# Performance work log

Hardware: AMD Instinct MI355X
Metric: run time of the kernel (lower is better)

Reference implementation:

```python
import jax, jax.numpy as jnp
import numpy as np

N = 50000   # nodes
E = 800000  # edges
H = 4       # heads
FH = 32     # hidden per head
C = 40      # classes
IN = 128    # input feats
EPS = 1e-5
NEG_SLOPE = 0.2


def setup_inputs() -> dict:
    key = jax.random.key(0)
    ks = jax.random.split(key, 32)
    rn = lambda k, s, sc=0.1: jax.random.normal(k, s, jnp.float32) * sc
    return {
        "feat": rn(ks[0], (N, IN), 1.0),
        "src": jax.random.randint(ks[1], (E,), 0, N, jnp.int32),
        "dst": jax.random.randint(ks[2], (E,), 0, N, jnp.int32),
        "w_fc0": rn(ks[3], (IN, H * FH)), "al0": rn(ks[4], (H, FH)), "ar0": rn(ks[5], (H, FH)),
        "b0": jnp.zeros((H * FH,), jnp.float32), "w_lin0": rn(ks[6], (IN, H * FH)),
        "g0": jnp.ones((H * FH,), jnp.float32), "be0": jnp.zeros((H * FH,), jnp.float32),
        "w_fc1": rn(ks[7], (H * FH, H * FH)), "al1": rn(ks[8], (H, FH)), "ar1": rn(ks[9], (H, FH)),
        "b1": jnp.zeros((H * FH,), jnp.float32), "w_lin1": rn(ks[10], (H * FH, H * FH)),
        "g1": jnp.ones((H * FH,), jnp.float32), "be1": jnp.zeros((H * FH,), jnp.float32),
        "w_fc2": rn(ks[11], (H * FH, H * C)), "al2": rn(ks[12], (H, C)), "ar2": rn(ks[13], (H, C)),
        "b2": jnp.zeros((H * C,), jnp.float32), "w_lin2": rn(ks[14], (H * FH, H * C)),
        "bias_last": jnp.zeros((C,), jnp.float32),
    }


def gat_layer(h, src, dst, w_fc, al, ar, b, w_lin, out_f):
    # h: [N, in]; ft: [N, H, out_f]
    ft = (h @ w_fc).reshape(N, H, out_f)
    el = jnp.einsum("nhf,hf->nh", ft, al)   # [N, H]
    er = jnp.einsum("nhf,hf->nh", ft, ar)   # [N, H]
    e = jax.nn.leaky_relu(el[src] + er[dst], NEG_SLOPE)  # [E, H]
    # segment softmax over destination neighborhoods
    m = jax.ops.segment_max(e, dst, num_segments=N)       # [N, H]
    ex = jnp.exp(e - m[dst])
    s = jax.ops.segment_sum(ex, dst, num_segments=N)      # [N, H]
    a = ex / s[dst]                                       # [E, H]
    msg = ft[src] * a[:, :, None]                         # [E, H, out_f]
    rst = jax.ops.segment_sum(msg, dst, num_segments=N)   # [N, H, out_f]
    rst = rst + b.reshape(1, H, out_f)
    skip = (h @ w_lin).reshape(N, H, out_f)
    return rst + skip


def batchnorm(x, g, be):
    mu = jnp.mean(x, axis=0)
    var = jnp.mean(jnp.square(x - mu), axis=0)
    return (x - mu) * jax.lax.rsqrt(var + EPS) * g + be


def reference(feat, src, dst,
              w_fc0, al0, ar0, b0, w_lin0, g0, be0,
              w_fc1, al1, ar1, b1, w_lin1, g1, be1,
              w_fc2, al2, ar2, b2, w_lin2, bias_last):
    h = feat
    h = gat_layer(h, src, dst, w_fc0, al0, ar0, b0, w_lin0, FH).reshape(N, H * FH)
    h = jax.nn.relu(batchnorm(h, g0, be0))
    h = gat_layer(h, src, dst, w_fc1, al1, ar1, b1, w_lin1, FH).reshape(N, H * FH)
    h = jax.nn.relu(batchnorm(h, g1, be1))
    h = gat_layer(h, src, dst, w_fc2, al2, ar2, b2, w_lin2, C)  # [N, H, C]
    h = h.mean(axis=1) + bias_last
    return jax.nn.log_softmax(h, axis=-1)
```

## Files before the change

kernel.cpp:

```cpp
#include <hip/hip_runtime.h>
#include <hip/hip_bf16.h>

#define GN 50000
#define GE 800000
#define GH 4
#define GFH 32
#define GC 40
#define GIN 128

typedef __hip_bfloat16 bf16;
typedef __attribute__((ext_vector_type(8))) short bf16x8;
typedef __attribute__((ext_vector_type(4))) float f32x4;

static __device__ __forceinline__ float ldx(const void* p, size_t i, int m) {
    if (m) return ((const float*)p)[i];
    return __bfloat162float(((const bf16*)p)[i]);
}
static __device__ __forceinline__ void stx(void* p, size_t i, int m, float v) {
    if (m) ((float*)p)[i] = v;
    else ((bf16*)p)[i] = __float2bfloat16(v);
}
static __device__ __forceinline__ unsigned short f2bfu(float v) {
    union { bf16 b; unsigned short u; } cv;
    cv.b = __float2bfloat16(v);
    return cv.u;
}
static __device__ __forceinline__ float lo16(unsigned u) { return __uint_as_float(u << 16); }
static __device__ __forceinline__ float hi16(unsigned u) { return __uint_as_float(u & 0xFFFF0000u); }
static __device__ __forceinline__ float guard_finite(float v) {
    if (!(v == v) || fabsf(v) > 1e30f) return 0.f;
    return v;
}

__global__ void detect_kernel(const unsigned short* __restrict__ f, int* __restrict__ flag) {
    int t = threadIdx.x;
    unsigned short u = f[t];
    int e = (u >> 7) & 0xFF;
    if (e >= 0x8E) atomicAdd(flag, 1);
}

__global__ void sentinel_kernel(unsigned short* __restrict__ o, int n) {
    int i = blockIdx.x * blockDim.x + threadIdx.x;
    if (i < n) o[i] = 0x3F80;
}

__global__ void count_kernel(const int* __restrict__ dst, int* __restrict__ deg, int n) {
    int e = blockIdx.x * blockDim.x + threadIdx.x;
    if (e < n) {
        int d = dst[e];
        if (d >= 0 && d < GN) atomicAdd(&deg[d], 1);
    }
}

__global__ void scan1_kernel(const int* __restrict__ deg, int* __restrict__ tmp,
                             int* __restrict__ bsum, int n) {
    int tid = threadIdx.x;
    int i = blockIdx.x * 256 + tid;
    int v = (i < n) ? deg[i] : 0;
    int lane = tid & 63, wid = tid >> 6;
    int s = v;
#pragma unroll
    for (int off = 1; off < 64; off <<= 1) {
        int u = __shfl_up(s, off);
        if (lane >= off) s += u;
    }
    __shared__ int wsum[4];
    if (lane == 63) wsum[wid] = s;
    __syncthreads();
    int woff = 0;
#pragma unroll
    for (int w = 0; w < 4; w++) woff += (w < wid) ? wsum[w] : 0;
    int incl = s + woff;
    if (i < n) tmp[i] = incl;
    if (tid == 255) bsum[blockIdx.x] = incl;
}

__global__ void scan2_kernel(int* __restrict__ bsum, int nb) {
    int tid = threadIdx.x;
    int v = (tid < nb) ? bsum[tid] : 0;
    int lane = tid & 63, wid = tid >> 6;
    int s = v;
#pragma unroll
    for (int off = 1; off < 64; off <<= 1) {
        int u = __shfl_up(s, off);
        if (lane >= off) s += u;
    }
    __shared__ int wsum[4];
    if (lane == 63) wsum[wid] = s;
    __syncthreads();
    int woff = 0;
#pragma unroll
    for (int w = 0; w < 4; w++) woff += (w < wid) ? wsum[w] : 0;
    if (tid < nb) bsum[tid] = s + woff - v;
}

__global__ void scan3_kernel(const int* __restrict__ deg, const int* __restrict__ tmp,
                             const int* __restrict__ bsum, int* __restrict__ indptr,
                             int* __restrict__ cursor, int n) {
    int i = blockIdx.x * 256 + threadIdx.x;
    if (i < n) {
        int incl = tmp[i] + bsum[blockIdx.x];
        indptr[i + 1] = incl;
        cursor[i] = incl - deg[i];
        if (i == 0) indptr[0] = 0;
    }
}

__global__ void scatter_kernel(const int* __restrict__ src, const int* __restrict__ dst,
                               int* __restrict__ cursor, int* __restrict__ csr_src, int n) {
    int e = blockIdx.x * blockDim.x + threadIdx.x;
    if (e < n) {
        int d = dst[e];
        if (d < 0 || d >= GN) return;
        int p = atomicAdd(&cursor[d], 1);
        if (p >= 0 && p < GE) csr_src[p] = src[e];
    }
}

__global__ void wmean_kernel(const void* __restrict__ w, unsigned short* __restrict__ wmt,
                             const int* __restrict__ flag) {
    int m = (*flag != 0) ? 1 : 0;
    int idx = blockIdx.x * blockDim.x + threadIdx.x;
    if (idx < 48 * 128) {
        int c = idx >> 7, k = idx & 127;
        float s = 0.f;
        if (c < 40) {
            s = 0.25f * (ldx(w, (size_t)k * 160 + c, m) + ldx(w, (size_t)k * 160 + 40 + c, m) +
                         ldx(w, (size_t)k * 160 + 80 + c, m) + ldx(w, (size_t)k * 160 + 120 + c, m));
        }
        wmt[c * 128 + k] = f2bfu(s);
    }
}

__global__ void wtrans_all(const void* __restrict__ wf0, const void* __restrict__ wl0,
                           const void* __restrict__ wf1, const void* __restrict__ wl1,
                           const void* __restrict__ wf2, unsigned short* __restrict__ tf0,
                           unsigned short* __restrict__ tl0, unsigned short* __restrict__ tf1,
                           unsigned short* __restrict__ tl1, unsigned short* __restrict__ tf2,
                           const int* __restrict__ flag) {
    int m = (*flag != 0) ? 1 : 0;
    int idx = blockIdx.x * blockDim.x + threadIdx.x;
    if (idx < 4 * 16384) {
        int which = idx >> 14, local = idx & 16383;
        const void* w = (which == 0) ? wf0 : (which == 1) ? wl0 : (which == 2) ? wf1 : wl1;
        unsigned short* t = (which == 0) ? tf0 : (which == 1) ? tl0 : (which == 2) ? tf1 : tl1;
        int c = local & 127, k = local >> 7;
        t[(size_t)c * 128 + k] = f2bfu(ldx(w, (size_t)k * 128 + c, m));
    } else if (idx < 4 * 16384 + 160 * 128) {
        int local = idx - 4 * 16384;
        int c = local % 160, k = local / 160;
        tf2[(size_t)c * 128 + k] = f2bfu(ldx(wf2, (size_t)k * 160 + c, m));
    }
}

__global__ void bn_coef(const float* __restrict__ gsum, const float* __restrict__ gsq,
                        const void* __restrict__ g, const void* __restrict__ be,
                        float* __restrict__ ka, float* __restrict__ kb, int n,
                        const int* __restrict__ flag) {
    int c = threadIdx.x;
    int m = (*flag != 0) ? 1 : 0;
    float inv_n = 1.f / (float)n;
    float mu = gsum[c] * inv_n;
    float var = gsq[c] * inv_n - mu * mu;
    float k = rsqrtf(fmaxf(var, 0.f) + 1e-5f) * ldx(g, c, m);
    ka[c] = k;
    kb[c] = ldx(be, c, m) - mu * k;
}

static __device__ __forceinline__ uint4 bnx8(uint4 v, int k0, const float* __restrict__ ka,
                                             const float* __restrict__ kb) {
    unsigned* pw = (unsigned*)&v;
#pragma unroll
    for (int j = 0; j < 4; j++) {
        int c = k0 + 2 * j;
        float y0 = fmaf(lo16(pw[j]), ka[c], kb[c]);
        float y1 = fmaf(hi16(pw[j]), ka[c + 1], kb[c + 1]);
        y0 = y0 > 0.f ? y0 : 0.f;
        y1 = y1 > 0.f ? y1 : 0.f;
        pw[j] = (unsigned)f2bfu(y0) | ((unsigned)f2bfu(y1) << 16);
    }
    return v;
}

__global__ __launch_bounds__(256) void gemm_dual(const void* __restrict__ X, int xext,
                                                 const unsigned short* __restrict__ WT1,
                                                 const unsigned short* __restrict__ WT2,
                                                 bf16* __restrict__ Y1, bf16* __restrict__ Y2,
                                                 int nrows, const float* __restrict__ ka,
                                                 const float* __restrict__ kb,
                                                 const void* __restrict__ al,
                                                 const void* __restrict__ ar,
                                                 float* __restrict__ elo,
                                                 float* __restrict__ ero,
                                                 const int* __restrict__ flag) {
    constexpr int LDX = 136;
    __shared__ unsigned short Xs[64 * LDX];
    __shared__ unsigned short Wt[128 * LDX];
    int m = (*flag != 0) ? 1 : 0;
    int xfp32 = xext && m;
    int tid = threadIdx.x;
    int rb = blockIdx.x * 64;

    if (xfp32) {
#pragma unroll
        for (int it = 0; it < 8; it++) {
            int e = (tid + it * 256) * 4;
            int r = e >> 7, k0 = e & 127;
            int row = rb + r;
            float4 v = {0.f, 0.f, 0.f, 0.f};
            if (row < nrows) v = *(const float4*)((const float*)X + (size_t)row * 128 + k0);
            unsigned lo = (unsigned)f2bfu(v.x) | ((unsigned)f2bfu(v.y) << 16);
            unsigned hi = (unsigned)f2bfu(v.z) | ((unsigned)f2bfu(v.w) << 16);
            uint2 o = {lo, hi};
            *(uint2*)&Xs[r * LDX + k0] = o;
        }
    } else {
#pragma unroll
        for (int it = 0; it < 4; it++) {
            int e = (tid + it * 256) * 8;
            int r = e >> 7, k0 = e & 127;
            int row = rb + r;
            uint4 v = {0u, 0u, 0u, 0u};
            if (row < nrows) v = *(const uint4*)((const unsigned short*)X + (size_t)row * 128 + k0);
            if (ka) v = bnx8(v, k0, ka, kb);
            *(uint4*)&Xs[r * LDX + k0] = v;
        }
    }
#pragma unroll
    for (int it = 0; it < 8; it++) {
        int e = (tid + it * 256) * 8;
        int c = e >> 7, k0 = e & 127;
        *(uint4*)&Wt[c * LDX + k0] = *(const uint4*)(WT1 + (size_t)c * 128 + k0);
    }
    __syncthreads();

    int wave = tid >> 6, lane = tid & 63;
    int lr = lane & 15, quad = lane >> 4;
    int mrow = wave * 16 + lr;
    int drow = rb + wave * 16 + quad * 4;

    {
        f32x4 acc[8] = {};
        for (int kk = 0; kk < 128; kk += 32) {
            bf16x8 a = *(const bf16x8*)&Xs[mrow * LDX + kk + quad * 8];
#pragma unroll
            for (int nt = 0; nt < 8; nt++) {
                bf16x8 b = *(const bf16x8*)&Wt[(nt * 16 + lr) * LDX + kk + quad * 8];
                acc[nt] = __builtin_amdgcn_mfma_f32_16x16x32_bf16(a, b, acc[nt], 0, 0, 0);
            }
        }
#pragma unroll
        for (int nt = 0; nt < 8; nt++) {
            int col = nt * 16 + lr;
#pragma unroll
            for (int i = 0; i < 4; i++) {
                int row = drow + i;
                if (row < nrows) Y1[(size_t)row * 128 + col] = __float2bfloat16(acc[nt][i]);
            }
        }
        float alv[8], arv[8];
#pragma unroll
        for (int nt = 0; nt < 8; nt++) {
            int c = nt * 16 + lr;
            alv[nt] = ldx(al, c, m);
            arv[nt] = ldx(ar, c, m);
        }
        float eo = 0.f, ro = 0.f;
#pragma unroll
        for (int i = 0; i < 4; i++) {
#pragma unroll
            for (int h = 0; h < 4; h++) {
                float es = acc[2 * h][i] * alv[2 * h] + acc[2 * h + 1][i] * alv[2 * h + 1];
                float rs = acc[2 * h][i] * arv[2 * h] + acc[2 * h + 1][i] * arv[2 * h + 1];
#pragma unroll
                for (int off = 1; off < 16; off <<= 1) {
                    es += __shfl_xor(es, off);
                    rs += __shfl_xor(rs, off);
                }
                bool mine = (lr == i * 4 + h);
                eo = mine ? es : eo;
                ro = mine ? rs : ro;
            }
        }
        int erow = drow + (lr >> 2);
        if (erow < nrows) {
            elo[(size_t)drow * 4 + lr] = eo;
            ero[(size_t)drow * 4 + lr] = ro;
        }
    }
    __syncthreads();
#pragma unroll
    for (int it = 0; it < 8; it++) {
        int e = (tid + it * 256) * 8;
        int c = e >> 7, k0 = e & 127;
        *(uint4*)&Wt[c * LDX + k0] = *(const uint4*)(WT2 + (size_t)c * 128 + k0);
    }
    __syncthreads();
    {
        f32x4 acc[8] = {};
        for (int kk = 0; kk < 128; kk += 32) {
            bf16x8 a = *(const bf16x8*)&Xs[mrow * LDX + kk + quad * 8];
#pragma unroll
            for (int nt = 0; nt < 8; nt++) {
                bf16x8 b = *(const bf16x8*)&Wt[(nt * 16 + lr) * LDX + kk + quad * 8];
                acc[nt] = __builtin_amdgcn_mfma_f32_16x16x32_bf16(a, b, acc[nt], 0, 0, 0);
            }
        }
#pragma unroll
        for (int nt = 0; nt < 8; nt++) {
            int col = nt * 16 + lr;
#pragma unroll
            for (int i = 0; i < 4; i++) {
                int row = drow + i;
                if (row < nrows) Y2[(size_t)row * 128 + col] = __float2bfloat16(acc[nt][i]);
            }
        }
    }
}

__global__ __launch_bounds__(256) void gemm_final(bf16* __restrict__ X,
                                                  const unsigned short* __restrict__ WT,
                                                  bf16* __restrict__ Y, int nrows,
                                                  const float* __restrict__ ka,
                                                  const float* __restrict__ kb) {
    constexpr int LDX = 136;
    __shared__ unsigned short Xs[64 * LDX];
    __shared__ unsigned short Wt[128 * LDX];
    int tid = threadIdx.x;
    int rb = blockIdx.x * 64;

#pragma unroll
    for (int it = 0; it < 4; it++) {
        int e = (tid + it * 256) * 8;
        int r = e >> 7, k0 = e & 127;
        int row = rb + r;
        uint4 v = {0u, 0u, 0u, 0u};
        if (row < nrows) v = *(const uint4*)((const unsigned short*)X + (size_t)row * 128 + k0);
        v = bnx8(v, k0, ka, kb);
        *(uint4*)&Xs[r * LDX + k0] = v;
    }
#pragma unroll
    for (int it = 0; it < 8; it++) {
        int e = (tid + it * 256) * 8;
        int c = e >> 7, k0 = e & 127;
        *(uint4*)&Wt[c * LDX + k0] = *(const uint4*)(WT + (size_t)c * 128 + k0);
    }
    __syncthreads();

    int wave = tid >> 6, lane = tid & 63;
    int lr = lane & 15, quad = lane >> 4;
    int mrow = wave * 16 + lr;
    int drow = rb + wave * 16 + quad * 4;

    {
        f32x4 acc[8] = {};
        for (int kk = 0; kk < 128; kk += 32) {
            bf16x8 a = *(const bf16x8*)&Xs[mrow * LDX + kk + quad * 8];
#pragma unroll
            for (int nt = 0; nt < 8; nt++) {
                bf16x8 b = *(const bf16x8*)&Wt[(nt * 16 + lr) * LDX + kk + quad * 8];
                acc[nt] = __builtin_amdgcn_mfma_f32_16x16x32_bf16(a, b, acc[nt], 0, 0, 0);
            }
        }
#pragma unroll
        for (int nt = 0; nt < 8; nt++) {
            int col = nt * 16 + lr;
#pragma unroll
            for (int i = 0; i < 4; i++) {
                int row = drow + i;
                if (row < nrows) Y[(size_t)row * 160 + col] = __float2bfloat16(acc[nt][i]);
            }
        }
    }
    __syncthreads();
#pragma unroll
    for (int it = 0; it < 5; it++) {
        int e = (tid + it * 256) * 8;
        int c = e >> 7, k0 = e & 127;
        *(uint4*)&Wt[c * LDX + k0] = *(const uint4*)(WT + (size_t)(128 + c) * 128 + k0);
    }
    __syncthreads();
    {
        f32x4 acc[5] = {};
        for (int kk = 0; kk < 128; kk += 32) {
            bf16x8 a = *(const bf16x8*)&Xs[mrow * LDX + kk + quad * 8];
#pragma unroll
            for (int nt = 0; nt < 5; nt++) {
                bf16x8 b = *(const bf16x8*)&Wt[(nt * 16 + lr) * LDX + kk + quad * 8];
                acc[nt] = __builtin_amdgcn_mfma_f32_16x16x32_bf16(a, b, acc[nt], 0, 0, 0);
            }
        }
#pragma unroll
        for (int nt = 0; nt < 5; nt++) {
            int colg = 128 + nt * 16 + lr;
#pragma unroll
            for (int i = 0; i < 4; i++) {
                int row = drow + i;
                if (row >= nrows) continue;
                if (colg < 160) {
                    Y[(size_t)row * 160 + colg] = __float2bfloat16(acc[nt][i]);
                } else {
                    int sc = colg - 160;
                    if (sc < 40) X[(size_t)row * 128 + sc] = __float2bfloat16(acc[nt][i]);
                }
            }
        }
    }
}

__global__ void elr_kernel(const bf16* __restrict__ ft, const void* __restrict__ al,
                           const void* __restrict__ ar, float* __restrict__ el,
                           float* __restrict__ er, int n, int F, const int* __restrict__ flag) {
    int m = (*flag != 0) ? 1 : 0;
    int gid = blockIdx.x * blockDim.x + threadIdx.x;
    if (gid >= n * 4) return;
    int nid = gid >> 2, h = gid & 3;
    const bf16* f = ft + (size_t)nid * (4 * F) + h * F;
    float sl = 0.f, sr = 0.f;
    for (int i0 = 0; i0 < F; i0 += 8) {
        bf16x8 v8 = *(const bf16x8*)(f + i0);
#pragma unroll
        for (int i = 0; i < 8; i++) {
            float v = __uint_as_float(((unsigned)(unsigned short)v8[i]) << 16);
            sl += v * ldx(al, h * F + i0 + i, m);
            sr += v * ldx(ar, h * F + i0 + i, m);
        }
    }
    el[gid] = sl;
    er[gid] = sr;
}

template <int FTOT, bool FINAL>
__global__ __launch_bounds__(256) void agg_wave(
    const bf16* __restrict__ ft, const float* __restrict__ el, const float* __restrict__ er,
    const int* __restrict__ indptr, const int* __restrict__ csr_src,
    const void* __restrict__ bias, const void* __restrict__ h_in,
    const bf16* __restrict__ skip_pre, bf16* __restrict__ out,
    const void* __restrict__ bias_last, void* __restrict__ fout,
    const int* __restrict__ flag) {
    constexpr int HF = FTOT / 4;
    int m = (*flag != 0) ? 1 : 0;
    int lane = threadIdx.x & 63;
    int v = blockIdx.x * 4 + (threadIdx.x >> 6);
    if (v >= GN) return;
    int beg = indptr[v], end = indptr[v + 1];
    beg = max(0, min(beg, GE));
    end = max(beg, min(end, GE));

    int h = lane & 3, jl = lane >> 2;
    int c0 = 2 * lane;
    int h0 = c0 / HF;
    float erv = er[v * 4 + h];

    float a0 = 0.f, a1 = 0.f, a2 = 0.f, a3 = 0.f;
    float s_part = 0.f;

    for (int cb = beg; cb < end; cb += 16) {
        int chn = end - cb;
        chn = chn < 16 ? chn : 16;
        int u = csr_src[cb + (jl < chn ? jl : chn - 1)];
        u = min(max(u, 0), GN - 1);
        float e = el[u * 4 + h] + erv;
        e = e > 0.f ? e : 0.2f * e;
        float w = (jl < chn) ? __expf(fminf(e, 60.f)) : 0.f;
        s_part += w;
#pragma unroll
        for (int jb = 0; jb < 16; jb += 8) {
            if (jb >= chn) break;
            unsigned pq[8];
            float wqv[8];
            unsigned pbq[8];
#pragma unroll
            for (int q = 0; q < 8; q++) {
                int j4 = (jb + q) * 4;
                int us = __builtin_amdgcn_readlane(u, j4);
                pq[q] = *(const unsigned*)(ft + (size_t)us * FTOT + c0);
                wqv[q] = __shfl(w, j4 + h0);
                if constexpr (FINAL) {
                    if (lane < 16) {
                        pbq[q] = *(const unsigned*)(ft + (size_t)us * FTOT + 128 + c0);
                    }
                }
            }
#pragma unroll
            for (int q = 0; q < 8; q++) {
                a0 += wqv[q] * lo16(pq[q]);
                a1 += wqv[q] * hi16(pq[q]);
                if constexpr (FINAL) {
                    float wb = __uint_as_float(
                        __builtin_amdgcn_readlane(__float_as_uint(w), (jb + q) * 4 + 3));
                    if (lane < 16) {
                        a2 += wb * lo16(pbq[q]);
                        a3 += wb * hi16(pbq[q]);
                    }
                }
            }
        }
    }

#pragma unroll
    for (int off = 4; off < 64; off <<= 1) s_part += __shfl_xor(s_part, off);
    float s0 = __shfl(s_part, h0);

    float r0 = (s0 > 0.f) ? a0 / s0 : 0.f;
    float r1 = (s0 > 0.f) ? a1 / s0 : 0.f;

    if constexpr (!FINAL) {
        unsigned pk = *(const unsigned*)(skip_pre + (size_t)v * FTOT + c0);
        float o0 = r0 + ldx(bias, c0, m) + lo16(pk);
        float o1 = r1 + ldx(bias, c0 + 1, m) + hi16(pk);
        unsigned po = ((unsigned)f2bfu(guard_finite(o1)) << 16) |
                      (unsigned)f2bfu(guard_finite(o0));
        *(unsigned*)(out + (size_t)v * FTOT + c0) = po;
    } else {
        float s3 = __shfl(s_part, 3);
        float o0 = r0 + ldx(bias, c0, m);
        float o1 = r1 + ldx(bias, c0 + 1, m);
        float r2 = (s3 > 0.f) ? a2 / s3 : 0.f;
        float r3 = (s3 > 0.f) ? a3 / s3 : 0.f;
        int cb0 = 128 + c0;
        float o2 = r2 + ldx(bias, (cb0 < FTOT) ? cb0 : 0, m);
        float o3 = r3 + ldx(bias, (cb0 + 1 < FTOT) ? cb0 + 1 : 1, m);

        int t = lane;
        bool od = (t & 1);
        int sA = (t >> 1) & 63;
        int sB = ((t + 40) >> 1) & 63;
        int sC = ((t + 80) >> 1) & 63;
        int sD1 = ((t + 120) >> 1) & 63;
        int sD2 = ((t >= 8 ? t - 8 : 0) >> 1);
        float vA0 = __shfl(o0, sA), vA1 = __shfl(o1, sA);
        float vB0 = __shfl(o0, sB), vB1 = __shfl(o1, sB);
        float vC0 = __shfl(o0, sC), vC1 = __shfl(o1, sC);
        float vD10 = __shfl(o0, sD1), vD11 = __shfl(o1, sD1);
        float vD20 = __shfl(o2, sD2), vD21 = __shfl(o3, sD2);
        float vA = od ? vA1 : vA0;
        float vB = od ? vB1 : vB0;
        float vC = od ? vC1 : vC0;
        float vD = (t < 8) ? (od ? vD11 : vD10) : (od ? vD21 : vD20);

        float x = -3.0e38f;
        if (t < 40) {
            float sm = __bfloat162float(((const bf16*)h_in)[(size_t)v * 128 + t]);
            x = 0.25f * (vA + vB + vC + vD) + sm + ldx(bias_last, t, m);
        }
        float mx = x;
#pragma unroll
        for (int off = 1; off < 64; off <<= 1) mx = fmaxf(mx, __shfl_xor(mx, off));
        float ex = (t < 40) ? __expf(x - mx) : 0.f;
        float sum = ex;
#pragma unroll
        for (int off = 1; off < 64; off <<= 1) sum += __shfl_xor(sum, off);
        if (t < 40) stx(fout, (size_t)v * 40 + t, m, guard_finite(x - mx - __logf(sum)));
    }
}

__global__ void bn_stats(const bf16* __restrict__ x, float* __restrict__ gsum,
                         float* __restrict__ gsq, int n) {
    __shared__ float ls[128], lq[128];
    int tid = threadIdx.x;
    if (tid < 128) {
        ls[tid] = 0.f;
        lq[tid] = 0.f;
    }
    __syncthreads();
    int rg = tid >> 4;
    int c8 = (tid & 15) * 8;
    int rows_per_block = (n + gridDim.x - 1) / gridDim.x;
    int r0 = blockIdx.x * rows_per_block;
    int r1 = min(n, r0 + rows_per_block);
    float s[8] = {}, q[8] = {};
    for (int r = r0 + rg; r < r1; r += 16) {
        uint4 v = *(const uint4*)((const unsigned short*)x + (size_t)r * 128 + c8);
        unsigned* pw = (unsigned*)&v;
#pragma unroll
        for (int i = 0; i < 4; i++) {
            float v0 = lo16(pw[i]), v1 = hi16(pw[i]);
            s[2 * i] += v0;
            q[2 * i] += v0 * v0;
            s[2 * i + 1] += v1;
            q[2 * i + 1] += v1 * v1;
        }
    }
#pragma unroll
    for (int i = 0; i < 8; i++) {
        atomicAdd(&ls[c8 + i], s[i]);
        atomicAdd(&lq[c8 + i], q[i]);
    }
    __syncthreads();
    if (tid < 128) {
        atomicAdd(&gsum[tid], ls[tid]);
        atomicAdd(&gsq[tid], lq[tid]);
    }
}

extern "C" void kernel_launch(void* const* d_in, const int* in_sizes, int n_in,
                              void* d_out, int out_size, void* d_ws, size_t ws_size,
                              hipStream_t stream) {
    const void* feat = d_in[0];
    const int* src = (const int*)d_in[1];
    const int* dst = (const int*)d_in[2];
    const void* w_fc0 = d_in[3];
    const void* al0 = d_in[4];
    const void* ar0 = d_in[5];
    const void* b0 = d_in[6];
    const void* w_lin0 = d_in[7];
    const void* g0 = d_in[8];
    const void* be0 = d_in[9];
    const void* w_fc1 = d_in[10];
    const void* al1 = d_in[11];
    const void* ar1 = d_in[12];
    const void* b1 = d_in[13];
    const void* w_lin1 = d_in[14];
    const void* g1 = d_in[15];
    const void* be1 = d_in[16];
    const void* w_fc2 = d_in[17];
    const void* al2 = d_in[18];
    const void* ar2 = d_in[19];
    const void* b2 = d_in[20];
    const void* w_lin2 = d_in[21];
    const void* bias_last = d_in[22];

    if (ws_size < 35000000) {
        sentinel_kernel<<<(out_size + 255) / 256, 256, 0, stream>>>((unsigned short*)d_out,
                                                                    out_size);
        return;
    }

    char* p = (char*)d_ws;
    auto alloc = [&](size_t bytes) {
        char* r = p;
        p += (bytes + 255) & ~(size_t)255;
        return r;
    };
    bf16* ftb = (bf16*)alloc((size_t)GN * 160 * 2);
    bf16* hbuf = (bf16*)alloc((size_t)GN * 128 * 2);
    float* elb = (float*)alloc((size_t)GN * 4 * 4);
    float* erb = (float*)alloc((size_t)GN * 4 * 4);
    int* indptr = (int*)alloc((size_t)(GN + 1) * 4);
    int* cursor = (int*)alloc((size_t)GN * 4);
    int* bsum = (int*)alloc(256 * 4);
    unsigned short* wtf0 = (unsigned short*)alloc(128 * 128 * 2);
    unsigned short* wtl0 = (unsigned short*)alloc(128 * 128 * 2);
    unsigned short* wtf1 = (unsigned short*)alloc(128 * 128 * 2);
    unsigned short* wtl1 = (unsigned short*)alloc(128 * 128 * 2);
    unsigned short* wtf2 = (unsigned short*)alloc(208 * 128 * 2);
    float* ka0 = (float*)alloc(128 * 4);
    float* kb0 = (float*)alloc(128 * 4);
    float* ka1 = (float*)alloc(128 * 4);
    float* kb1 = (float*)alloc(128 * 4);
    char* zbase = p;
    int* deg = (int*)alloc((size_t)GN * 4);
    int* csr = (int*)alloc((size_t)GE * 4);
    float* gs0 = (float*)alloc(128 * 4);
    float* gq0 = (float*)alloc(128 * 4);
    float* gs1 = (float*)alloc(128 * 4);
    float* gq1 = (float*)alloc(128 * 4);
    int* flag = (int*)alloc(4);
    hipMemsetAsync(zbase, 0, (size_t)(p - zbase), stream);

    unsigned short* wmt = wtf2 + 160 * 128;

    detect_kernel<<<1, 256, 0, stream>>>((const unsigned short*)feat, flag);

    const int NB = (GN + 255) / 256;
    count_kernel<<<(GE + 255) / 256, 256, 0, stream>>>(dst, deg, GE);
    scan1_kernel<<<NB, 256, 0, stream>>>(deg, cursor, bsum, GN);
    scan2_kernel<<<1, 256, 0, stream>>>(bsum, NB);
    scan3_kernel<<<NB, 256, 0, stream>>>(deg, cursor, bsum, indptr, cursor, GN);
    scatter_kernel<<<(GE + 255) / 256, 256, 0, stream>>>(src, dst, cursor, csr, GE);
    wmean_kernel<<<24, 256, 0, stream>>>(w_lin2, wmt, flag);
    wtrans_all<<<(4 * 16384 + 160 * 128 + 255) / 256, 256, 0, stream>>>(
        w_fc0, w_lin0, w_fc1, w_lin1, w_fc2, wtf0, wtl0, wtf1, wtl1, wtf2, flag);

    const int AGGB = (GN + 3) / 4;

    gemm_dual<<<782, 256, 0, stream>>>(feat, 1, wtf0, wtl0, ftb, hbuf, GN, nullptr, nullptr,
                                       al0, ar0, elb, erb, flag);
    agg_wave<128, false><<<AGGB, 256, 0, stream>>>(ftb, elb, erb, indptr, csr, b0, nullptr,
                                                   hbuf, hbuf, nullptr, nullptr, flag);
    bn_stats<<<256, 256, 0, stream>>>(hbuf, gs0, gq0, GN);
    bn_coef<<<1, 128, 0, stream>>>(gs0, gq0, g0, be0, ka0, kb0, GN, flag);

    gemm_dual<<<782, 256, 0, stream>>>(hbuf, 0, wtf1, wtl1, ftb, hbuf, GN, ka0, kb0,
                                       al1, ar1, elb, erb, flag);
    agg_wave<128, false><<<AGGB, 256, 0, stream>>>(ftb, elb, erb, indptr, csr, b1, nullptr,
                                                   hbuf, hbuf, nullptr, nullptr, flag);
    bn_stats<<<256, 256, 0, stream>>>(hbuf, gs1, gq1, GN);
    bn_coef<<<1, 128, 0, stream>>>(gs1, gq1, g1, be1, ka1, kb1, GN, flag);

    gemm_final<<<782, 256, 0, stream>>>(hbuf, wtf2, ftb, GN, ka1, kb1);
    elr_kernel<<<(GN * 4 + 255) / 256, 256, 0, stream>>>(ftb, al2, ar2, elb, erb, GN, 40, flag);
    agg_wave<160, true><<<AGGB, 256, 0, stream>>>(ftb, elb, erb, indptr, csr, b2, hbuf,
                                                  nullptr, nullptr, bias_last, d_out, flag);
}
```

Baseline: 440.6 us.

## Fold small kernels together, preconvert features, and prefetch GEMM weights into registers

Merges the w_lin2 mean computation into the weight transpose kernel. Folds the BatchNorm coefficient computation into bn_stats with a last-block-done counter, removing separate tiny launches. Adds a standalone feature-to-bf16 conversion kernel written into ftb, so gemm_dual always reads bf16 input. Both GEMMs now issue all X and weight global loads into registers up front before the LDS stores, which overlaps load latency at the cost of higher register pressure and an extra pass over the features.

```diff
diff --git a/kernel.cpp b/kernel.cpp
--- a/kernel.cpp
+++ b/kernel.cpp
@@ -42,6 +42,26 @@
 __global__ void sentinel_kernel(unsigned short* __restrict__ o, int n) {
     int i = blockIdx.x * blockDim.x + threadIdx.x;
     if (i < n) o[i] = 0x3F80;
+}
+
+__global__ void featcvt_kernel(const void* __restrict__ f, unsigned short* __restrict__ o,
+                               const int* __restrict__ flag) {
+    int m = (*flag != 0) ? 1 : 0;
+    size_t base = ((size_t)blockIdx.x * blockDim.x + threadIdx.x) * 8;
+    if (base >= (size_t)GN * 128) return;
+    if (m) {
+        const float* fp = (const float*)f + base;
+        float4 a = *(const float4*)fp;
+        float4 b = *(const float4*)(fp + 4);
+        uint4 ov;
+        ov.x = (unsigned)f2bfu(a.x) | ((unsigned)f2bfu(a.y) << 16);
+        ov.y = (unsigned)f2bfu(a.z) | ((unsigned)f2bfu(a.w) << 16);
+        ov.z = (unsigned)f2bfu(b.x) | ((unsigned)f2bfu(b.y) << 16);
+        ov.w = (unsigned)f2bfu(b.z) | ((unsigned)f2bfu(b.w) << 16);
+        *(uint4*)(o + base) = ov;
+    } else {
+        *(uint4*)(o + base) = *(const uint4*)((const unsigned short*)f + base);
+    }
 }
 
 __global__ void count_kernel(const int* __restrict__ dst, int* __restrict__ deg, int n) {
@@ -117,27 +137,12 @@
     }
 }
 
-__global__ void wmean_kernel(const void* __restrict__ w, unsigned short* __restrict__ wmt,
-                             const int* __restrict__ flag) {
-    int m = (*flag != 0) ? 1 : 0;
-    int idx = blockIdx.x * blockDim.x + threadIdx.x;
-    if (idx < 48 * 128) {
-        int c = idx >> 7, k = idx & 127;
-        float s = 0.f;
-        if (c < 40) {
-            s = 0.25f * (ldx(w, (size_t)k * 160 + c, m) + ldx(w, (size_t)k * 160 + 40 + c, m) +
-                         ldx(w, (size_t)k * 160 + 80 + c, m) + ldx(w, (size_t)k * 160 + 120 + c, m));
-        }
-        wmt[c * 128 + k] = f2bfu(s);
-    }
-}
-
 __global__ void wtrans_all(const void* __restrict__ wf0, const void* __restrict__ wl0,
                            const void* __restrict__ wf1, const void* __restrict__ wl1,
-                           const void* __restrict__ wf2, unsigned short* __restrict__ tf0,
-                           unsigned short* __restrict__ tl0, unsigned short* __restrict__ tf1,
-                           unsigned short* __restrict__ tl1, unsigned short* __restrict__ tf2,
-                           const int* __restrict__ flag) {
+                           const void* __restrict__ wf2, const void* __restrict__ wl2,
+                           unsigned short* __restrict__ tf0, unsigned short* __restrict__ tl0,
+                           unsigned short* __restrict__ tf1, unsigned short* __restrict__ tl1,
+                           unsigned short* __restrict__ tf2, const int* __restrict__ flag) {
     int m = (*flag != 0) ? 1 : 0;
     int idx = blockIdx.x * blockDim.x + threadIdx.x;
     if (idx < 4 * 16384) {
@@ -150,21 +155,17 @@
         int local = idx - 4 * 16384;
         int c = local % 160, k = local / 160;
         tf2[(size_t)c * 128 + k] = f2bfu(ldx(wf2, (size_t)k * 160 + c, m));
-    }
-}
-
-__global__ void bn_coef(const float* __restrict__ gsum, const float* __restrict__ gsq,
-                        const void* __restrict__ g, const void* __restrict__ be,
-                        float* __restrict__ ka, float* __restrict__ kb, int n,
-                        const int* __restrict__ flag) {
-    int c = threadIdx.x;
-    int m = (*flag != 0) ? 1 : 0;
-    float inv_n = 1.f / (float)n;
-    float mu = gsum[c] * inv_n;
-    float var = gsq[c] * inv_n - mu * mu;
-    float k = rsqrtf(fmaxf(var, 0.f) + 1e-5f) * ldx(g, c, m);
-    ka[c] = k;
-    kb[c] = ldx(be, c, m) - mu * k;
+    } else if (idx < 4 * 16384 + 160 * 128 + 48 * 128) {
+        int local = idx - 4 * 16384 - 160 * 128;
+        int c = local >> 7, k = local & 127;
+        float s = 0.f;
+        if (c < 40) {
+            s = 0.25f * (ldx(wl2, (size_t)k * 160 + c, m) + ldx(wl2, (size_t)k * 160 + 40 + c, m) +
+                         ldx(wl2, (size_t)k * 160 + 80 + c, m) +
+                         ldx(wl2, (size_t)k * 160 + 120 + c, m));
+        }
+        tf2[(size_t)(160 + c) * 128 + k] = f2bfu(s);
+    }
 }
 
 static __device__ __forceinline__ uint4 bnx8(uint4 v, int k0, const float* __restrict__ ka,
@@ -182,7 +183,7 @@
     return v;
 }
 
-__global__ __launch_bounds__(256) void gemm_dual(const void* __restrict__ X, int xext,
+__global__ __launch_bounds__(256) void gemm_dual(const bf16* __restrict__ X,
                                                  const unsigned short* __restrict__ WT1,
                                                  const unsigned short* __restrict__ WT2,
                                                  bf16* __restrict__ Y1, bf16* __restrict__ Y2,
@@ -197,40 +198,46 @@
     __shared__ unsigned short Xs[64 * LDX];
     __shared__ unsigned short Wt[128 * LDX];
     int m = (*flag != 0) ? 1 : 0;
-    int xfp32 = xext && m;
     int tid = threadIdx.x;
     int rb = blockIdx.x * 64;
 
-    if (xfp32) {
-#pragma unroll
-        for (int it = 0; it < 8; it++) {
-            int e = (tid + it * 256) * 4;
-            int r = e >> 7, k0 = e & 127;
-            int row = rb + r;
-            float4 v = {0.f, 0.f, 0.f, 0.f};
-            if (row < nrows) v = *(const float4*)((const float*)X + (size_t)row * 128 + k0);
-            unsigned lo = (unsigned)f2bfu(v.x) | ((unsigned)f2bfu(v.y) << 16);
-            unsigned hi = (unsigned)f2bfu(v.z) | ((unsigned)f2bfu(v.w) << 16);
-            uint2 o = {lo, hi};
-            *(uint2*)&Xs[r * LDX + k0] = o;
-        }
-    } else {
-#pragma unroll
-        for (int it = 0; it < 4; it++) {
-            int e = (tid + it * 256) * 8;
-            int r = e >> 7, k0 = e & 127;
-            int row = rb + r;
-            uint4 v = {0u, 0u, 0u, 0u};
-            if (row < nrows) v = *(const uint4*)((const unsigned short*)X + (size_t)row * 128 + k0);
-            if (ka) v = bnx8(v, k0, ka, kb);
-            *(uint4*)&Xs[r * LDX + k0] = v;
-        }
-    }
+    uint4 xv[4];
+#pragma unroll
+    for (int it = 0; it < 4; it++) {
+        int e = (tid + it * 256) * 8;
+        int r = e >> 7, k0 = e & 127;
+        int row = rb + r;
+        uint4 v = {0u, 0u, 0u, 0u};
+        if (row < nrows) v = *(const uint4*)((const unsigned short*)X + (size_t)row * 128 + k0);
+        xv[it] = v;
+    }
+    uint4 w1v[8];
 #pragma unroll
     for (int it = 0; it < 8; it++) {
         int e = (tid + it * 256) * 8;
         int c = e >> 7, k0 = e & 127;
-        *(uint4*)&Wt[c * LDX + k0] = *(const uint4*)(WT1 + (size_t)c * 128 + k0);
+        w1v[it] = *(const uint4*)(WT1 + (size_t)c * 128 + k0);
+    }
+    uint4 w2v[8];
+#pragma unroll
+    for (int it = 0; it < 8; it++) {
+        int e = (tid + it * 256) * 8;
+        int c = e >> 7, k0 = e & 127;
+        w2v[it] = *(const uint4*)(WT2 + (size_t)c * 128 + k0);
+    }
+#pragma unroll
+    for (int it = 0; it < 4; it++) {
+        int e = (tid + it * 256) * 8;
+        int r = e >> 7, k0 = e & 127;
+        uint4 v = xv[it];
+        if (ka) v = bnx8(v, k0, ka, kb);
+        *(uint4*)&Xs[r * LDX + k0] = v;
+    }
+#pragma unroll
+    for (int it = 0; it < 8; it++) {
+        int e = (tid + it * 256) * 8;
+        int c = e >> 7, k0 = e & 127;
+        *(uint4*)&Wt[c * LDX + k0] = w1v[it];
     }
     __syncthreads();
 
@@ -293,7 +300,7 @@
     for (int it = 0; it < 8; it++) {
         int e = (tid + it * 256) * 8;
         int c = e >> 7, k0 = e & 127;
-        *(uint4*)&Wt[c * LDX + k0] = *(const uint4*)(WT2 + (size_t)c * 128 + k0);
+        *(uint4*)&Wt[c * LDX + k0] = w2v[it];
     }
     __syncthreads();
     {
@@ -329,6 +336,7 @@
     int tid = threadIdx.x;
     int rb = blockIdx.x * 64;
 
+    uint4 xv[4];
 #pragma unroll
     for (int it = 0; it < 4; it++) {
         int e = (tid + it * 256) * 8;
@@ -336,14 +344,33 @@
         int row = rb + r;
         uint4 v = {0u, 0u, 0u, 0u};
         if (row < nrows) v = *(const uint4*)((const unsigned short*)X + (size_t)row * 128 + k0);
-        v = bnx8(v, k0, ka, kb);
-        *(uint4*)&Xs[r * LDX + k0] = v;
-    }
+        xv[it] = v;
+    }
+    uint4 w1v[8];
 #pragma unroll
     for (int it = 0; it < 8; it++) {
         int e = (tid + it * 256) * 8;
         int c = e >> 7, k0 = e & 127;
-        *(uint4*)&Wt[c * LDX + k0] = *(const uint4*)(WT + (size_t)c * 128 + k0);
+        w1v[it] = *(const uint4*)(WT + (size_t)c * 128 + k0);
+    }
+    uint4 w2v[5];
+#pragma unroll
+    for (int it = 0; it < 5; it++) {
+        int e = (tid + it * 256) * 8;
+        int c = e >> 7, k0 = e & 127;
+        w2v[it] = *(const uint4*)(WT + (size_t)(128 + c) * 128 + k0);
+    }
+#pragma unroll
+    for (int it = 0; it < 4; it++) {
+        int e = (tid + it * 256) * 8;
+        int r = e >> 7, k0 = e & 127;
+        *(uint4*)&Xs[r * LDX + k0] = bnx8(xv[it], k0, ka, kb);
+    }
+#pragma unroll
+    for (int it = 0; it < 8; it++) {
+        int e = (tid + it * 256) * 8;
+        int c = e >> 7, k0 = e & 127;
+        *(uint4*)&Wt[c * LDX + k0] = w1v[it];
     }
     __syncthreads();
 
@@ -377,7 +404,7 @@
     for (int it = 0; it < 5; it++) {
         int e = (tid + it * 256) * 8;
         int c = e >> 7, k0 = e & 127;
-        *(uint4*)&Wt[c * LDX + k0] = *(const uint4*)(WT + (size_t)(128 + c) * 128 + k0);
+        *(uint4*)&Wt[c * LDX + k0] = w2v[it];
     }
     __syncthreads();
     {
@@ -556,8 +583,12 @@
 }
 
 __global__ void bn_stats(const bf16* __restrict__ x, float* __restrict__ gsum,
-                         float* __restrict__ gsq, int n) {
+                         float* __restrict__ gsq, int n, const void* __restrict__ g,
+                         const void* __restrict__ be, float* __restrict__ ka,
+                         float* __restrict__ kb, int* __restrict__ done,
+                         const int* __restrict__ flag) {
     __shared__ float ls[128], lq[128];
+    __shared__ int lastv;
     int tid = threadIdx.x;
     if (tid < 128) {
         ls[tid] = 0.f;
@@ -591,6 +622,21 @@
     if (tid < 128) {
         atomicAdd(&gsum[tid], ls[tid]);
         atomicAdd(&gsq[tid], lq[tid]);
+    }
+    __threadfence();
+    __syncthreads();
+    if (tid == 0) lastv = (atomicAdd(done, 1) == (int)gridDim.x - 1) ? 1 : 0;
+    __syncthreads();
+    if (lastv && tid < 128) {
+        int m = (*flag != 0) ? 1 : 0;
+        float sv = atomicAdd(&gsum[tid], 0.f);
+        float qv = atomicAdd(&gsq[tid], 0.f);
+        float inv_n = 1.f / (float)n;
+        float mu = sv * inv_n;
+        float var = qv * inv_n - mu * mu;
+        float k = rsqrtf(fmaxf(var, 0.f) + 1e-5f) * ldx(g, tid, m);
+        ka[tid] = k;
+        kb[tid] = ldx(be, tid, m) - mu * k;
     }
 }
 
@@ -656,10 +702,10 @@
     float* gq0 = (float*)alloc(128 * 4);
     float* gs1 = (float*)alloc(128 * 4);
     float* gq1 = (float*)alloc(128 * 4);
+    int* done0 = (int*)alloc(4);
+    int* done1 = (int*)alloc(4);
     int* flag = (int*)alloc(4);
     hipMemsetAsync(zbase, 0, (size_t)(p - zbase), stream);
-
-    unsigned short* wmt = wtf2 + 160 * 128;
 
     detect_kernel<<<1, 256, 0, stream>>>((const unsigned short*)feat, flag);
 
@@ -669,25 +715,24 @@
     scan2_kernel<<<1, 256, 0, stream>>>(bsum, NB);
     scan3_kernel<<<NB, 256, 0, stream>>>(deg, cursor, bsum, indptr, cursor, GN);
     scatter_kernel<<<(GE + 255) / 256, 256, 0, stream>>>(src, dst, cursor, csr, GE);
-    wmean_kernel<<<24, 256, 0, stream>>>(w_lin2, wmt, flag);
-    wtrans_all<<<(4 * 16384 + 160 * 128 + 255) / 256, 256, 0, stream>>>(
-        w_fc0, w_lin0, w_fc1, w_lin1, w_fc2, wtf0, wtl0, wtf1, wtl1, wtf2, flag);
+    wtrans_all<<<(4 * 16384 + 160 * 128 + 48 * 128 + 255) / 256, 256, 0, stream>>>(
+        w_fc0, w_lin0, w_fc1, w_lin1, w_fc2, w_lin2, wtf0, wtl0, wtf1, wtl1, wtf2, flag);
+    featcvt_kernel<<<(GN * 128 / 8 + 255) / 256, 256, 0, stream>>>(
+        feat, (unsigned short*)ftb, flag);
 
     const int AGGB = (GN + 3) / 4;
 
-    gemm_dual<<<782, 256, 0, stream>>>(feat, 1, wtf0, wtl0, ftb, hbuf, GN, nullptr, nullptr,
+    gemm_dual<<<782, 256, 0, stream>>>(ftb, wtf0, wtl0, ftb, hbuf, GN, nullptr, nullptr,
                                        al0, ar0, elb, erb, flag);
     agg_wave<128, false><<<AGGB, 256, 0, stream>>>(ftb, elb, erb, indptr, csr, b0, nullptr,
                                                    hbuf, hbuf, nullptr, nullptr, flag);
-    bn_stats<<<256, 256, 0, stream>>>(hbuf, gs0, gq0, GN);
-    bn_coef<<<1, 128, 0, stream>>>(gs0, gq0, g0, be0, ka0, kb0, GN, flag);
-
-    gemm_dual<<<782, 256, 0, stream>>>(hbuf, 0, wtf1, wtl1, ftb, hbuf, GN, ka0, kb0,
+    bn_stats<<<256, 256, 0, stream>>>(hbuf, gs0, gq0, GN, g0, be0, ka0, kb0, done0, flag);
+
+    gemm_dual<<<782, 256, 0, stream>>>(hbuf, wtf1, wtl1, ftb, hbuf, GN, ka0, kb0,
                                        al1, ar1, elb, erb, flag);
     agg_wave<128, false><<<AGGB, 256, 0, stream>>>(ftb, elb, erb, indptr, csr, b1, nullptr,
                                                    hbuf, hbuf, nullptr, nullptr, flag);
-    bn_stats<<<256, 256, 0, stream>>>(hbuf, gs1, gq1, GN);
-    bn_coef<<<1, 128, 0, stream>>>(gs1, gq1, g1, be1, ka1, kb1, GN, flag);
+    bn_stats<<<256, 256, 0, stream>>>(hbuf, gs1, gq1, GN, g1, be1, ka1, kb1, done1, flag);
 
     gemm_final<<<782, 256, 0, stream>>>(hbuf, wtf2, ftb, GN, ka1, kb1);
     elr_kernel<<<(GN * 4 + 255) / 256, 256, 0, stream>>>(ftb, al2, ar2, elb, erb, GN, 40, flag);
```

New measurement: 475.3 us. 1.08x slower.

## Build CSR via two-pass bucketed scatter to localize atomic writes

Applied to the files above, without the earlier changes.

Replaces the direct per-edge scatter into CSR with a two-pass bucketing scheme. Edges are first grouped into 64 coarse destination buckets using shared-memory histograms, then each bucket's range is scattered into the final CSR, so cursor atomics and writes stay within a small region. The w_lin2 mean-weight kernel is also folded into the weight-transpose launch. In exchange this adds kernels and an extra pass over the edges, uses ftb as temporary buffers, and makes edge order inside a node nondeterministic.

```diff
diff --git a/kernel.cpp b/kernel.cpp
--- a/kernel.cpp
+++ b/kernel.cpp
@@ -44,12 +44,26 @@
     if (i < n) o[i] = 0x3F80;
 }
 
-__global__ void count_kernel(const int* __restrict__ dst, int* __restrict__ deg, int n) {
-    int e = blockIdx.x * blockDim.x + threadIdx.x;
-    if (e < n) {
-        int d = dst[e];
-        if (d >= 0 && d < GN) atomicAdd(&deg[d], 1);
-    }
+__global__ void count_kernel(const int* __restrict__ dst, int* __restrict__ deg,
+                             int* __restrict__ bcnt, int n) {
+    __shared__ int h[64];
+    int tid = threadIdx.x;
+    if (tid < 64) h[tid] = 0;
+    __syncthreads();
+    int base = blockIdx.x * 4096;
+#pragma unroll
+    for (int j = 0; j < 16; j++) {
+        int e = base + j * 256 + tid;
+        if (e < n) {
+            int d = dst[e];
+            if (d >= 0 && d < GN) {
+                atomicAdd(&deg[d], 1);
+                atomicAdd(&h[d >> 10], 1);
+            }
+        }
+    }
+    __syncthreads();
+    if (tid < 64 && h[tid]) atomicAdd(&bcnt[tid], h[tid]);
 }
 
 __global__ void scan1_kernel(const int* __restrict__ deg, int* __restrict__ tmp,
@@ -106,38 +120,80 @@
     }
 }
 
-__global__ void scatter_kernel(const int* __restrict__ src, const int* __restrict__ dst,
-                               int* __restrict__ cursor, int* __restrict__ csr_src, int n) {
-    int e = blockIdx.x * blockDim.x + threadIdx.x;
-    if (e < n) {
-        int d = dst[e];
-        if (d < 0 || d >= GN) return;
+__global__ void bucket_scan(const int* __restrict__ bcnt, int* __restrict__ boff,
+                            int* __restrict__ bcur) {
+    int tid = threadIdx.x;
+    int v = bcnt[tid];
+    int s = v;
+#pragma unroll
+    for (int off = 1; off < 64; off <<= 1) {
+        int u = __shfl_up(s, off);
+        if (tid >= off) s += u;
+    }
+    boff[tid + 1] = s;
+    bcur[tid] = s - v;
+    if (tid == 0) boff[0] = 0;
+}
+
+__global__ void bucket_scatter(const int* __restrict__ src, const int* __restrict__ dst,
+                               int* __restrict__ bcur, int* __restrict__ bsrc,
+                               int* __restrict__ bdst, int n) {
+    __shared__ int h[64], gbase[64];
+    int tid = threadIdx.x;
+    if (tid < 64) h[tid] = 0;
+    __syncthreads();
+    int base = blockIdx.x * 4096;
+    int s_[16], d_[16];
+    int cnt = 0;
+#pragma unroll
+    for (int j = 0; j < 16; j++) {
+        int e = base + j * 256 + tid;
+        if (e < n) {
+            int dd = dst[e];
+            if (dd >= 0 && dd < GN) {
+                s_[cnt] = src[e];
+                d_[cnt] = dd;
+                cnt++;
+                atomicAdd(&h[dd >> 10], 1);
+            }
+        }
+    }
+    __syncthreads();
+    if (tid < 64) gbase[tid] = h[tid] ? atomicAdd(&bcur[tid], h[tid]) : 0;
+    __syncthreads();
+    if (tid < 64) h[tid] = 0;
+    __syncthreads();
+    for (int j = 0; j < cnt; j++) {
+        int b = d_[j] >> 10;
+        int loc = atomicAdd(&h[b], 1);
+        int pos = gbase[b] + loc;
+        bsrc[pos] = s_[j];
+        bdst[pos] = d_[j];
+    }
+}
+
+__global__ void bucket_final(const int* __restrict__ bsrc, const int* __restrict__ bdst,
+                             const int* __restrict__ boff, int* __restrict__ cursor,
+                             int* __restrict__ csr) {
+    int b = blockIdx.x >> 3;
+    int sub = blockIdx.x & 7;
+    int s0 = boff[b], s1 = boff[b + 1];
+    int len = s1 - s0;
+    int beg = s0 + (int)(((long long)len * sub) >> 3);
+    int end = s0 + (int)(((long long)len * (sub + 1)) >> 3);
+    for (int i = beg + threadIdx.x; i < end; i += 256) {
+        int d = bdst[i];
         int p = atomicAdd(&cursor[d], 1);
-        if (p >= 0 && p < GE) csr_src[p] = src[e];
-    }
-}
-
-__global__ void wmean_kernel(const void* __restrict__ w, unsigned short* __restrict__ wmt,
-                             const int* __restrict__ flag) {
-    int m = (*flag != 0) ? 1 : 0;
-    int idx = blockIdx.x * blockDim.x + threadIdx.x;
-    if (idx < 48 * 128) {
-        int c = idx >> 7, k = idx & 127;
-        float s = 0.f;
-        if (c < 40) {
-            s = 0.25f * (ldx(w, (size_t)k * 160 + c, m) + ldx(w, (size_t)k * 160 + 40 + c, m) +
-                         ldx(w, (size_t)k * 160 + 80 + c, m) + ldx(w, (size_t)k * 160 + 120 + c, m));
-        }
-        wmt[c * 128 + k] = f2bfu(s);
+        if (p >= 0 && p < GE) csr[p] = bsrc[i];
     }
 }
 
 __global__ void wtrans_all(const void* __restrict__ wf0, const void* __restrict__ wl0,
                            const void* __restrict__ wf1, const void* __restrict__ wl1,
-                           const void* __restrict__ wf2, unsigned short* __restrict__ tf0,
-                           unsigned short* __restrict__ tl0, unsigned short* __restrict__ tf1,
-                           unsigned short* __restrict__ tl1, unsigned short* __restrict__ tf2,
-                           const int* __restrict__ flag) {
+                           const void* __restrict__ wf2, const void* __restrict__ wl2,
+                           unsigned short* __restrict__ tf0, unsigned short* __restrict__ tl0,
+                           unsigned short* __restrict__ tf1, unsigned short* __restrict__ tl1,
+                           unsigned short* __restrict__ tf2, const int* __restrict__ flag) {
     int m = (*flag != 0) ? 1 : 0;
     int idx = blockIdx.x * blockDim.x + threadIdx.x;
     if (idx < 4 * 16384) {
@@ -150,6 +206,16 @@
         int local = idx - 4 * 16384;
         int c = local % 160, k = local / 160;
         tf2[(size_t)c * 128 + k] = f2bfu(ldx(wf2, (size_t)k * 160 + c, m));
+    } else if (idx < 4 * 16384 + 160 * 128 + 48 * 128) {
+        int local = idx - 4 * 16384 - 160 * 128;
+        int c = local >> 7, k = local & 127;
+        float s = 0.f;
+        if (c < 40) {
+            s = 0.25f * (ldx(wl2, (size_t)k * 160 + c, m) + ldx(wl2, (size_t)k * 160 + 40 + c, m) +
+                         ldx(wl2, (size_t)k * 160 + 80 + c, m) +
+                         ldx(wl2, (size_t)k * 160 + 120 + c, m));
+        }
+        tf2[(size_t)(160 + c) * 128 + k] = f2bfu(s);
     }
 }
 
@@ -656,22 +722,28 @@
     float* gq0 = (float*)alloc(128 * 4);
     float* gs1 = (float*)alloc(128 * 4);
     float* gq1 = (float*)alloc(128 * 4);
+    int* bcnt = (int*)alloc(64 * 4);
+    int* boff = (int*)alloc(72 * 4);
+    int* bcur = (int*)alloc(64 * 4);
     int* flag = (int*)alloc(4);
     hipMemsetAsync(zbase, 0, (size_t)(p - zbase), stream);
 
-    unsigned short* wmt = wtf2 + 160 * 128;
+    int* bsrc = (int*)ftb;
+    int* bdst = bsrc + GE;
 
     detect_kernel<<<1, 256, 0, stream>>>((const unsigned short*)feat, flag);
 
     const int NB = (GN + 255) / 256;
-    count_kernel<<<(GE + 255) / 256, 256, 0, stream>>>(dst, deg, GE);
+    const int EB = (GE + 4095) / 4096;
+    count_kernel<<<EB, 256, 0, stream>>>(dst, deg, bcnt, GE);
+    bucket_scan<<<1, 64, 0, stream>>>(bcnt, boff, bcur);
     scan1_kernel<<<NB, 256, 0, stream>>>(deg, cursor, bsum, GN);
     scan2_kernel<<<1, 256, 0, stream>>>(bsum, NB);
     scan3_kernel<<<NB, 256, 0, stream>>>(deg, cursor, bsum, indptr, cursor, GN);
-    scatter_kernel<<<(GE + 255) / 256, 256, 0, stream>>>(src, dst, cursor, csr, GE);
-    wmean_kernel<<<24, 256, 0, stream>>>(w_lin2, wmt, flag);
-    wtrans_all<<<(4 * 16384 + 160 * 128 + 255) / 256, 256, 0, stream>>>(
-        w_fc0, w_lin0, w_fc1, w_lin1, w_fc2, wtf0, wtl0, wtf1, wtl1, wtf2, flag);
+    bucket_scatter<<<EB, 256, 0, stream>>>(src, dst, bcur, bsrc, bdst, GE);
+    bucket_final<<<64 * 8, 256, 0, stream>>>(bsrc, bdst, boff, cursor, csr);
+    wtrans_all<<<(4 * 16384 + 160 * 128 + 48 * 128 + 255) / 256, 256, 0, stream>>>(
+        w_fc0, w_lin0, w_fc1, w_lin1, w_fc2, w_lin2, wtf0, wtl0, wtf1, wtl1, wtf2, flag);
 
     const int AGGB = (GN + 3) / 4;
 
```

After: 447.6 us. About the same (+1.6%).
